# Performance work log

Hardware: AMD Instinct MI355X
Metric: run time of the kernel (lower is better)

## Reference

```python
import jax, jax.numpy as jnp
import numpy as np
import math

B, T, C, H = 2, 2048, 1024, 16
HD = C // H  # head_dim = 64


def _rope_cos_sin(t, hd, base=10000.0):
    inv_freq = 1.0 / (base ** (jnp.arange(0, hd, 2, dtype=jnp.float32) / hd))
    freqs = jnp.arange(t, dtype=jnp.float32)[:, None] * inv_freq[None, :]  # [T, hd//2]
    emb = jnp.concatenate([freqs, freqs], axis=-1)  # [T, hd]
    return jnp.cos(emb)[None, None], jnp.sin(emb)[None, None]  # [1,1,T,hd]


def setup_inputs() -> dict:
    key = jax.random.key(0)
    k1, k2, k3 = jax.random.split(key, 3)
    x = jax.random.normal(k1, (B, T, C), dtype=jnp.float32)
    W_attn = jax.random.normal(k2, (C, 3 * C), dtype=jnp.float32) * (1.0 / math.sqrt(C))
    W_proj = jax.random.normal(k3, (C, C), dtype=jnp.float32) * (1.0 / math.sqrt(C))
    mask = jnp.tril(jnp.ones((T, T), dtype=bool))[None, None]  # causal [1,1,T,T]
    return {"x": x, "W_attn": W_attn, "W_proj": W_proj, "mask": mask}


def reference(x, W_attn, W_proj, mask):
    b, t, c = x.shape
    qkv = x @ W_attn  # [B,T,3C]
    q, k, v = jnp.split(qkv, 3, axis=-1)
    q = q.reshape(b, t, H, HD).transpose(0, 2, 1, 3)  # [B,H,T,HD]
    k = k.reshape(b, t, H, HD).transpose(0, 2, 1, 3)
    v = v.reshape(b, t, H, HD).transpose(0, 2, 1, 3)
    cos, sin = _rope_cos_sin(t, HD)
    # roll-based RoPE: x*cos + roll(x, 1, axis=-1)*sin
    q = q * cos + jnp.roll(q, 1, axis=-1) * sin
    k = k * cos + jnp.roll(k, 1, axis=-1) * sin
    scale = 1.0 / math.sqrt(HD)
    att = jnp.einsum('bhqd,bhkd->bhqk', q, k) * scale  # [B,H,T,T]
    att = jnp.where(mask, att, -jnp.inf)
    att = jax.nn.softmax(att, axis=-1)
    y = jnp.einsum('bhqk,bhkd->bhqd', att, v)
    y = y.transpose(0, 2, 1, 3).reshape(b, t, c)
    return y @ W_proj
```

## Files before the change

### kernel.cpp

```cpp
#include <hip/hip_runtime.h>


typedef __attribute__((ext_vector_type(8))) short short8;
typedef __attribute__((ext_vector_type(4))) float floatx4;

__device__ __forceinline__ ushort f2bf(float f) {
    unsigned x = __float_as_uint(f);
    x += 0x7fffu + ((x >> 16) & 1u);
    return (ushort)(x >> 16);
}
__device__ __forceinline__ float bf2f(ushort u) {
    return __uint_as_float(((unsigned)u) << 16);
}
__device__ __forceinline__ float exp2fast(float x) {
    float r;
    asm("v_exp_f32 %0, %1" : "=v"(r) : "v"(x));
    return r;
}
__device__ __forceinline__ unsigned cvtpk_bf16(float lo, float hi) {
    unsigned r;
    asm("v_cvt_pk_bf16_f32 %0, %1, %2" : "=v"(r) : "v"(lo), "v"(hi));
    return r;
}

#define MFMA16(a, b, c) __builtin_amdgcn_mfma_f32_16x16x32_bf16((a), (b), (c), 0, 0, 0)

__device__ __forceinline__ void glds16(const ushort* g, ushort* l) {
    __builtin_amdgcn_global_load_lds(
        (const __attribute__((address_space(1))) unsigned int*)g,
        (__attribute__((address_space(3))) unsigned int*)l, 16, 0, 0);
}

__global__ __launch_bounds__(256) void tp_k(const float* __restrict__ src,
                                            ushort* __restrict__ dst,
                                            int R, int C) {
    __shared__ ushort t[32][34];
    const int c0 = blockIdx.x * 32, r0 = blockIdx.y * 32;
    const int tr = threadIdx.x >> 5, tc = threadIdx.x & 31;
#pragma unroll
    for (int j = 0; j < 4; j++)
        t[tr + j * 8][tc] = f2bf(src[(size_t)(r0 + tr + j * 8) * C + c0 + tc]);
    __syncthreads();
#pragma unroll
    for (int j = 0; j < 4; j++)
        dst[(size_t)(c0 + tr + j * 8) * R + r0 + tc] = t[tc][tr + j * 8];
}

__global__ __launch_bounds__(256) void cvt_k(const float* __restrict__ src,
                                             ushort* __restrict__ dst) {
    const size_t i = ((size_t)blockIdx.x * 256 + threadIdx.x) * 4;
    float4 t4 = *(const float4*)&src[i];
    *(ushort4*)&dst[i] = make_ushort4(f2bf(t4.x), f2bf(t4.y), f2bf(t4.z), f2bf(t4.w));
}

__global__ __launch_bounds__(256) void trig_k(float2* __restrict__ tab) {
    const int idx = blockIdx.x * 256 + threadIdx.x;
    const int t = idx >> 5, j = idx & 31;
    const double inv = pow(10000.0, -(double)j / 32.0);
    const double ang = (double)t * inv;
    tab[idx] = make_float2((float)cos(ang), (float)sin(ang));
}

__global__ __launch_bounds__(256, 3) void gemm1_qkv_k(const ushort* __restrict__ Ab,
                                                      const ushort* __restrict__ Bt,
                                                      ushort* __restrict__ qb,
                                                      ushort* __restrict__ kb,
                                                      ushort* __restrict__ vtb) {
    __shared__ __align__(16) ushort As[128 * 64];
    __shared__ __align__(16) ushort Bs[128 * 64];
    const size_t boff = (size_t)blockIdx.z * (2048u * 1024u);
    Ab += boff; qb += boff; kb += boff; vtb += boff;
    const int tid = threadIdx.x;
    const int m0 = blockIdx.y * 128, n0 = blockIdx.x * 128;
    const int w = tid >> 6, lane = tid & 63, quad = lane >> 4, l16 = lane & 15;
    const int wr = w >> 1, wc = w & 1;
    const int K = 1024;
    const int srow = lane >> 3, sslot = lane & 7;

    floatx4 acc[4][4];
#pragma unroll
    for (int mt = 0; mt < 4; mt++)
#pragma unroll
        for (int nt = 0; nt < 4; nt++) acc[mt][nt] = (floatx4){0.f, 0.f, 0.f, 0.f};

    for (int k0 = 0; k0 < K; k0 += 64) {
        __syncthreads();
#pragma unroll
        for (int jj = 0; jj < 4; jj++) {
            const int reg = jj * 4 + w;
            const int row = reg * 8 + srow;
            const int cs = sslot ^ (row & 7);
            glds16(&Ab[(size_t)(m0 + row) * K + k0 + cs * 8], &As[reg * 512]);
        }
#pragma unroll
        for (int jj = 0; jj < 4; jj++) {
            const int reg = jj * 4 + w;
            const int row = reg * 8 + srow;
            const int cs = sslot ^ (row & 7);
            glds16(&Bt[(size_t)(n0 + row) * K + k0 + cs * 8], &Bs[reg * 512]);
        }
        __syncthreads();

#pragma unroll
        for (int kk = 0; kk < 2; kk++) {
            short8 af[4], bfr[4];
#pragma unroll
            for (int mt = 0; mt < 4; mt++) {
                const int row = wr * 64 + mt * 16 + l16;
                const int slot = ((kk << 2) | quad) ^ (row & 7);
                af[mt] = *(short8*)&As[row * 64 + slot * 8];
            }
#pragma unroll
            for (int nt = 0; nt < 4; nt++) {
                const int row = wc * 64 + nt * 16 + l16;
                const int slot = ((kk << 2) | quad) ^ (row & 7);
                bfr[nt] = *(short8*)&Bs[row * 64 + slot * 8];
            }
#pragma unroll
            for (int mt = 0; mt < 4; mt++)
#pragma unroll
                for (int nt = 0; nt < 4; nt++) acc[mt][nt] = MFMA16(af[mt], bfr[nt], acc[mt][nt]);
        }
    }

#pragma unroll
    for (int nt = 0; nt < 4; nt++) {
        const int n = n0 + wc * 64 + nt * 16 + l16;
        const int seg = n >> 10;
        const int cn = n & 1023;
        const int h = cn >> 6, d = cn & 63;
#pragma unroll
        for (int mt = 0; mt < 4; mt++) {
#pragma unroll
            for (int r = 0; r < 4; r++) {
                const int t = m0 + wr * 64 + mt * 16 + quad * 4 + r;
                const ushort v = f2bf(acc[mt][nt][r]);
                if (seg == 0)      qb[((size_t)h * 2048 + t) * 64 + d] = v;
                else if (seg == 1) kb[((size_t)h * 2048 + t) * 64 + d] = v;
                else               vtb[((size_t)h * 64 + d) * 2048 + t] = v;
            }
        }
    }
}

__global__ __launch_bounds__(256) void rope_k(ushort* __restrict__ q,
                                              ushort* __restrict__ k,
                                              const float2* __restrict__ tab) {
    const int wid = blockIdx.x * 4 + (threadIdx.x >> 6);
    const int lane = threadIdx.x & 63;
    const int t = wid & 2047;
    const float2 cs = tab[t * 32 + (lane & 31)];
    const float c = cs.x;
    const float s = cs.y;
    const size_t base = (size_t)wid * 64;

    float qv = bf2f(q[base + lane]);
    float qp = __shfl(qv, (lane + 63) & 63, 64);
    q[base + lane] = f2bf(qv * c + qp * s);

    float kv = bf2f(k[base + lane]);
    float kp = __shfl(kv, (lane + 63) & 63, 64);
    k[base + lane] = f2bf(kv * c + kp * s);
}

__global__ __launch_bounds__(256, 2) void attn_k(const ushort* __restrict__ q,
                                                 const ushort* __restrict__ k,
                                                 const ushort* __restrict__ vt,
                                                 ushort* __restrict__ y) {
    __shared__ __align__(16) ushort Ks[128 * 64];
    __shared__ __align__(16) ushort Vs[64 * 128];
    __shared__ __align__(16) ushort Ps[4][16][136];

    const int bid = blockIdx.x;
    const int b = bid >> 9;
    const int r9 = bid & 511;
    const int qt = (r9 < 256) ? (31 - (r9 >> 4)) : ((r9 >> 4) - 16);
    const int h = r9 & 15;
    const size_t boff = (size_t)b * (2048u * 1024u);
    q += boff; k += boff; vt += boff; y += boff;
    const int tid = threadIdx.x, w = tid >> 6, lane = tid & 63;
    const int quad = lane >> 4, l16 = lane & 15;
    const int srow8 = lane >> 3, sslot8 = lane & 7;
    const int srow4 = lane >> 4, sslot16 = lane & 15;

    const int q0 = qt * 64;
    const int qrow = q0 + w * 16 + l16;
    const int wrow0 = q0 + w * 16;
    const int nkt = (qt >> 1) + 1;
    const float SC = 0.125f * 1.44269504f;

    short8 qa0, qa1;
    {
        const ushort* qp = q + ((size_t)h * 2048 + qrow) * 64 + quad * 8;
        qa0 = *(const short8*)(qp);
        qa1 = *(const short8*)(qp + 32);
    }

    floatx4 O[4];
#pragma unroll
    for (int dt = 0; dt < 4; dt++) O[dt] = (floatx4){0.f, 0.f, 0.f, 0.f};
    float M = -30000.f, L = 0.f;

    for (int kt2 = 0; kt2 < nkt; kt2++) {
        const int kbase = kt2 * 128;
        __syncthreads();
#pragma unroll
        for (int jj = 0; jj < 4; jj++) {
            const int reg = jj * 4 + w;
            const int row = reg * 8 + srow8;
            const int cs = sslot8 ^ (row & 7);
            glds16(&k[((size_t)h * 2048 + kbase + row) * 64 + cs * 8], &Ks[reg * 512]);
        }
#pragma unroll
        for (int jj = 0; jj < 4; jj++) {
            const int reg = jj * 4 + w;
            const int row = reg * 4 + srow4;
            const int cs = sslot16 ^ (row & 15);
            glds16(&vt[((size_t)h * 64 + row) * 2048 + kbase + cs * 8], &Vs[reg * 512]);
        }
        __syncthreads();

        floatx4 s[8];
        __builtin_amdgcn_s_setprio(1);
#pragma unroll
        for (int nt = 0; nt < 8; nt++) {
            const int row = nt * 16 + l16;
            short8 ka0 = *(short8*)&Ks[row * 64 + ((quad ^ (row & 7)) * 8)];
            short8 ka1 = *(short8*)&Ks[row * 64 + (((4 | quad) ^ (row & 7)) * 8)];
            floatx4 z = (floatx4){0.f, 0.f, 0.f, 0.f};
            z = MFMA16(ka0, qa0, z);
            z = MFMA16(ka1, qa1, z);
            s[nt] = z;
        }
        __builtin_amdgcn_s_setprio(0);

        if (kbase + 127 <= wrow0) {
#pragma unroll
            for (int nt = 0; nt < 8; nt++)
#pragma unroll
                for (int r = 0; r < 4; r++) s[nt][r] *= SC;
        } else {
#pragma unroll
            for (int nt = 0; nt < 8; nt++)
#pragma unroll
                for (int r = 0; r < 4; r++) {
                    const int kidx = kbase + nt * 16 + quad * 4 + r;
                    const float vv = s[nt][r] * SC;
                    s[nt][r] = (kidx > qrow) ? -30000.f : vv;
                }
        }

        float mr[8];
#pragma unroll
        for (int nt = 0; nt < 8; nt++)
            mr[nt] = fmaxf(fmaxf(s[nt][0], s[nt][1]), fmaxf(s[nt][2], s[nt][3]));
        float mx = fmaxf(fmaxf(fmaxf(mr[0], mr[1]), fmaxf(mr[2], mr[3])),
                         fmaxf(fmaxf(mr[4], mr[5]), fmaxf(mr[6], mr[7])));
        mx = fmaxf(mx, __shfl_xor(mx, 16, 64));
        mx = fmaxf(mx, __shfl_xor(mx, 32, 64));

        if (!__all(mx <= M)) {
            const float Mn = fmaxf(M, mx);
            const float alpha = exp2fast(M - Mn);
            L *= alpha;
#pragma unroll
            for (int dt = 0; dt < 4; dt++) O[dt] *= alpha;
            M = Mn;
        }

        float sum = 0.f;
#pragma unroll
        for (int nt = 0; nt < 8; nt++)
#pragma unroll
            for (int r = 0; r < 4; r++) {
                const float pv = exp2fast(s[nt][r] - M);
                s[nt][r] = pv;
                sum += pv;
            }
        sum += __shfl_xor(sum, 16, 64);
        sum += __shfl_xor(sum, 32, 64);
        L += sum;

#pragma unroll
        for (int nt = 0; nt < 8; nt++) {
            uint2 pk2;
            pk2.x = cvtpk_bf16(s[nt][0], s[nt][1]);
            pk2.y = cvtpk_bf16(s[nt][2], s[nt][3]);
            *(uint2*)&Ps[w][l16][nt * 16 + quad * 4] = pk2;
        }

        short8 pb[4];
#pragma unroll
        for (int ks = 0; ks < 4; ks++)
            pb[ks] = *(short8*)&Ps[w][l16][ks * 32 + quad * 8];
        __builtin_amdgcn_s_setprio(1);
#pragma unroll
        for (int dt = 0; dt < 4; dt++) {
            const int row = dt * 16 + l16;
#pragma unroll
            for (int ks = 0; ks < 4; ks++) {
                const int cc = (ks * 4 + quad) ^ (row & 15);
                short8 va = *(short8*)&Vs[row * 128 + cc * 8];
                O[dt] = MFMA16(va, pb[ks], O[dt]);
            }
        }
        __builtin_amdgcn_s_setprio(0);
    }

    const float rl = 1.0f / L;
#pragma unroll
    for (int dt = 0; dt < 4; dt++) {
        ushort4 o4 = make_ushort4(f2bf(O[dt][0] * rl), f2bf(O[dt][1] * rl),
                                  f2bf(O[dt][2] * rl), f2bf(O[dt][3] * rl));
        *(ushort4*)&y[(size_t)qrow * 1024 + h * 64 + dt * 16 + quad * 4] = o4;
    }
}

__global__ __launch_bounds__(256, 2) void gemm2_proj_k(const ushort* __restrict__ Y,
                                                       const ushort* __restrict__ Bt,
                                                       float* __restrict__ out) {
    __shared__ __align__(16) ushort As[64 * 64];
    __shared__ __align__(16) ushort Bs[64 * 64];
    const size_t boff = (size_t)blockIdx.z * (2048u * 1024u);
    Y += boff; out += boff;
    const int tid = threadIdx.x;
    const int m0 = blockIdx.y * 64, n0 = blockIdx.x * 64;
    const int w = tid >> 6, lane = tid & 63, quad = lane >> 4, l16 = lane & 15;
    const int wr = w >> 1, wc = w & 1;
    const int K = 1024;
    const int srow = lane >> 3, sslot = lane & 7;

    floatx4 acc[2][2];
#pragma unroll
    for (int mt = 0; mt < 2; mt++)
#pragma unroll
        for (int nt = 0; nt < 2; nt++) acc[mt][nt] = (floatx4){0.f, 0.f, 0.f, 0.f};

    for (int k0 = 0; k0 < K; k0 += 64) {
        __syncthreads();
#pragma unroll
        for (int jj = 0; jj < 2; jj++) {
            const int reg = jj * 4 + w;
            const int row = reg * 8 + srow;
            const int cs = sslot ^ (row & 7);
            glds16(&Y[(size_t)(m0 + row) * K + k0 + cs * 8], &As[reg * 512]);
            glds16(&Bt[(size_t)(n0 + row) * K + k0 + cs * 8], &Bs[reg * 512]);
        }
        __syncthreads();

#pragma unroll
        for (int kk = 0; kk < 2; kk++) {
            short8 af[2], bfr[2];
#pragma unroll
            for (int mt = 0; mt < 2; mt++) {
                const int row = wr * 32 + mt * 16 + l16;
                const int slot = ((kk << 2) | quad) ^ (row & 7);
                af[mt] = *(short8*)&As[row * 64 + slot * 8];
            }
#pragma unroll
            for (int nt = 0; nt < 2; nt++) {
                const int row = wc * 32 + nt * 16 + l16;
                const int slot = ((kk << 2) | quad) ^ (row & 7);
                bfr[nt] = *(short8*)&Bs[row * 64 + slot * 8];
            }
#pragma unroll
            for (int mt = 0; mt < 2; mt++)
#pragma unroll
                for (int nt = 0; nt < 2; nt++) acc[mt][nt] = MFMA16(af[mt], bfr[nt], acc[mt][nt]);
        }
    }

#pragma unroll
    for (int mt = 0; mt < 2; mt++)
#pragma unroll
        for (int nt = 0; nt < 2; nt++) {
            const int n = n0 + wc * 32 + nt * 16 + l16;
#pragma unroll
            for (int r = 0; r < 4; r++) {
                const int m = m0 + wr * 32 + mt * 16 + quad * 4 + r;
                out[(size_t)m * 1024 + n] = acc[mt][nt][r];
            }
        }
}

extern "C" void kernel_launch(void* const* d_in, const int* in_sizes, int n_in,
                              void* d_out, int out_size, void* d_ws, size_t ws_size,
                              hipStream_t stream) {
    const float* x  = (const float*)d_in[0];
    const float* Wa = (const float*)d_in[1];
    const float* Wp = (const float*)d_in[2];
    float* out = (float*)d_out;

    const size_t PB = (size_t)2048 * 1024;
    ushort* wtA = (ushort*)(out + PB);
    float2* tab = (float2*)(wtA + (size_t)3 * 1024 * 1024);

    if (ws_size >= (size_t)36 * 1024 * 1024) {
        ushort* qbA = (ushort*)d_ws;
        ushort* kbA = qbA + 2 * PB;
        ushort* vtA = qbA + 4 * PB;
        ushort* ybA = qbA + 6 * PB;
        ushort* wtP = qbA + 8 * PB;

        tp_k<<<dim3(96, 32), 256, 0, stream>>>(Wa, wtA, 1024, 3072);
        trig_k<<<dim3(256), 256, 0, stream>>>(tab);
        tp_k<<<dim3(32, 32), 256, 0, stream>>>(Wp, wtP, 1024, 1024);

        cvt_k<<<dim3(4096), 256, 0, stream>>>(x, ybA);
        gemm1_qkv_k<<<dim3(24, 16, 2), 256, 0, stream>>>(ybA, wtA, qbA, kbA, vtA);
        rope_k<<<dim3(16384), 256, 0, stream>>>(qbA, kbA, tab);
        attn_k<<<dim3(1024), 256, 0, stream>>>(qbA, kbA, vtA, ybA);
        gemm2_proj_k<<<dim3(16, 32, 2), 256, 0, stream>>>(ybA, wtP, out);
        return;
    }

    ushort* qb  = (ushort*)d_ws;
    ushort* kb  = qb + PB;
    ushort* vtb = kb + PB;
    ushort* yb  = vtb + PB;
    const bool hoistWp = ws_size >= (size_t)18 * 1024 * 1024;
    ushort* wtP_stable = yb + PB;

    tp_k<<<dim3(96, 32), 256, 0, stream>>>(Wa, wtA, 1024, 3072);
    trig_k<<<dim3(256), 256, 0, stream>>>(tab);
    if (hoistWp)
        tp_k<<<dim3(32, 32), 256, 0, stream>>>(Wp, wtP_stable, 1024, 1024);

    for (int b = 0; b < 2; b++) {
        cvt_k<<<dim3(2048), 256, 0, stream>>>(x + b * PB, yb);
        gemm1_qkv_k<<<dim3(24, 16, 1), 256, 0, stream>>>(yb, wtA, qb, kb, vtb);
        rope_k<<<dim3(8192), 256, 0, stream>>>(qb, kb, tab);
        attn_k<<<dim3(512), 256, 0, stream>>>(qb, kb, vtb, yb);
        if (hoistWp) {
            gemm2_proj_k<<<dim3(16, 32, 1), 256, 0, stream>>>(yb, wtP_stable, out + b * PB);
        } else {
            tp_k<<<dim3(32, 32), 256, 0, stream>>>(Wp, qb, 1024, 1024);
            gemm2_proj_k<<<dim3(16, 32, 1), 256, 0, stream>>>(yb, qb, out + b * PB);
        }
    }
}
```

Baseline: 204.1 us.

## Pair complementary causal query tiles per attention block to share K/V loads

Each attention workgroup now handles two query tiles, a late tile (31-g) and an early tile (g). Every K/V tile staged in shared memory is reused for both, and each block does a balanced amount of causal work. This halves the grid and cuts redundant K/V global loads for the early tile. In exchange it doubles the per-thread accumulator and Q registers, which may lower occupancy, and leaves fewer blocks (512) across the device's CUs.

```diff
diff --git a/kernel.cpp b/kernel.cpp
--- a/kernel.cpp
+++ b/kernel.cpp
@@ -172,10 +172,11 @@
     __shared__ __align__(16) ushort Ps[4][16][136];
 
     const int bid = blockIdx.x;
-    const int b = bid >> 9;
-    const int r9 = bid & 511;
-    const int qt = (r9 < 256) ? (31 - (r9 >> 4)) : ((r9 >> 4) - 16);
-    const int h = r9 & 15;
+    const int b = bid >> 8;
+    const int r8 = bid & 255;
+    const int g = r8 >> 4;
+    const int h = r8 & 15;
+    const int qtA = 31 - g, qtB = g;
     const size_t boff = (size_t)b * (2048u * 1024u);
     q += boff; k += boff; vt += boff; y += boff;
     const int tid = threadIdx.x, w = tid >> 6, lane = tid & 63;
@@ -183,25 +184,33 @@
     const int srow8 = lane >> 3, sslot8 = lane & 7;
     const int srow4 = lane >> 4, sslot16 = lane & 15;
 
-    const int q0 = qt * 64;
-    const int qrow = q0 + w * 16 + l16;
-    const int wrow0 = q0 + w * 16;
-    const int nkt = (qt >> 1) + 1;
+    const int qrowA = qtA * 64 + w * 16 + l16;
+    const int qrowB = qtB * 64 + w * 16 + l16;
+    const int wrow0A = qtA * 64 + w * 16;
+    const int wrow0B = qtB * 64 + w * 16;
+    const int nktA = (qtA >> 1) + 1;
+    const int nktB = (qtB >> 1) + 1;
     const float SC = 0.125f * 1.44269504f;
 
-    short8 qa0, qa1;
+    short8 qaA0, qaA1, qaB0, qaB1;
     {
-        const ushort* qp = q + ((size_t)h * 2048 + qrow) * 64 + quad * 8;
-        qa0 = *(const short8*)(qp);
-        qa1 = *(const short8*)(qp + 32);
-    }
-
-    floatx4 O[4];
-#pragma unroll
-    for (int dt = 0; dt < 4; dt++) O[dt] = (floatx4){0.f, 0.f, 0.f, 0.f};
-    float M = -30000.f, L = 0.f;
-
-    for (int kt2 = 0; kt2 < nkt; kt2++) {
+        const ushort* qp = q + ((size_t)h * 2048 + qrowA) * 64 + quad * 8;
+        qaA0 = *(const short8*)(qp);
+        qaA1 = *(const short8*)(qp + 32);
+        const ushort* qp2 = q + ((size_t)h * 2048 + qrowB) * 64 + quad * 8;
+        qaB0 = *(const short8*)(qp2);
+        qaB1 = *(const short8*)(qp2 + 32);
+    }
+
+    floatx4 OA[4], OB[4];
+#pragma unroll
+    for (int dt = 0; dt < 4; dt++) {
+        OA[dt] = (floatx4){0.f, 0.f, 0.f, 0.f};
+        OB[dt] = (floatx4){0.f, 0.f, 0.f, 0.f};
+    }
+    float MA = -30000.f, LA = 0.f, MB = -30000.f, LB = 0.f;
+
+    for (int kt2 = 0; kt2 < nktA; kt2++) {
         const int kbase = kt2 * 128;
         __syncthreads();
 #pragma unroll
@@ -220,99 +229,198 @@
         }
         __syncthreads();
 
-        floatx4 s[8];
-        __builtin_amdgcn_s_setprio(1);
-#pragma unroll
-        for (int nt = 0; nt < 8; nt++) {
-            const int row = nt * 16 + l16;
-            short8 ka0 = *(short8*)&Ks[row * 64 + ((quad ^ (row & 7)) * 8)];
-            short8 ka1 = *(short8*)&Ks[row * 64 + (((4 | quad) ^ (row & 7)) * 8)];
-            floatx4 z = (floatx4){0.f, 0.f, 0.f, 0.f};
-            z = MFMA16(ka0, qa0, z);
-            z = MFMA16(ka1, qa1, z);
-            s[nt] = z;
-        }
-        __builtin_amdgcn_s_setprio(0);
-
-        if (kbase + 127 <= wrow0) {
+        {
+            floatx4 s[8];
+            __builtin_amdgcn_s_setprio(1);
+#pragma unroll
+            for (int nt = 0; nt < 8; nt++) {
+                const int row = nt * 16 + l16;
+                short8 ka0 = *(short8*)&Ks[row * 64 + ((quad ^ (row & 7)) * 8)];
+                short8 ka1 = *(short8*)&Ks[row * 64 + (((4 | quad) ^ (row & 7)) * 8)];
+                floatx4 z = (floatx4){0.f, 0.f, 0.f, 0.f};
+                z = MFMA16(ka0, qaA0, z);
+                z = MFMA16(ka1, qaA1, z);
+                s[nt] = z;
+            }
+            __builtin_amdgcn_s_setprio(0);
+
+            if (kbase + 127 <= wrow0A) {
+#pragma unroll
+                for (int nt = 0; nt < 8; nt++)
+#pragma unroll
+                    for (int r = 0; r < 4; r++) s[nt][r] *= SC;
+            } else {
+#pragma unroll
+                for (int nt = 0; nt < 8; nt++)
+#pragma unroll
+                    for (int r = 0; r < 4; r++) {
+                        const int kidx = kbase + nt * 16 + quad * 4 + r;
+                        const float vv = s[nt][r] * SC;
+                        s[nt][r] = (kidx > qrowA) ? -30000.f : vv;
+                    }
+            }
+
+            float mr[8];
 #pragma unroll
             for (int nt = 0; nt < 8; nt++)
-#pragma unroll
-                for (int r = 0; r < 4; r++) s[nt][r] *= SC;
-        } else {
+                mr[nt] = fmaxf(fmaxf(s[nt][0], s[nt][1]), fmaxf(s[nt][2], s[nt][3]));
+            float mx = fmaxf(fmaxf(fmaxf(mr[0], mr[1]), fmaxf(mr[2], mr[3])),
+                             fmaxf(fmaxf(mr[4], mr[5]), fmaxf(mr[6], mr[7])));
+            mx = fmaxf(mx, __shfl_xor(mx, 16, 64));
+            mx = fmaxf(mx, __shfl_xor(mx, 32, 64));
+
+            if (!__all(mx <= MA)) {
+                const float Mn = fmaxf(MA, mx);
+                const float alpha = exp2fast(MA - Mn);
+                LA *= alpha;
+#pragma unroll
+                for (int dt = 0; dt < 4; dt++) OA[dt] *= alpha;
+                MA = Mn;
+            }
+
+            float sum = 0.f;
 #pragma unroll
             for (int nt = 0; nt < 8; nt++)
 #pragma unroll
                 for (int r = 0; r < 4; r++) {
-                    const int kidx = kbase + nt * 16 + quad * 4 + r;
-                    const float vv = s[nt][r] * SC;
-                    s[nt][r] = (kidx > qrow) ? -30000.f : vv;
+                    const float pv = exp2fast(s[nt][r] - MA);
+                    s[nt][r] = pv;
+                    sum += pv;
                 }
-        }
-
-        float mr[8];
-#pragma unroll
-        for (int nt = 0; nt < 8; nt++)
-            mr[nt] = fmaxf(fmaxf(s[nt][0], s[nt][1]), fmaxf(s[nt][2], s[nt][3]));
-        float mx = fmaxf(fmaxf(fmaxf(mr[0], mr[1]), fmaxf(mr[2], mr[3])),
-                         fmaxf(fmaxf(mr[4], mr[5]), fmaxf(mr[6], mr[7])));
-        mx = fmaxf(mx, __shfl_xor(mx, 16, 64));
-        mx = fmaxf(mx, __shfl_xor(mx, 32, 64));
-
-        if (!__all(mx <= M)) {
-            const float Mn = fmaxf(M, mx);
-            const float alpha = exp2fast(M - Mn);
-            L *= alpha;
-#pragma unroll
-            for (int dt = 0; dt < 4; dt++) O[dt] *= alpha;
-            M = Mn;
-        }
-
-        float sum = 0.f;
-#pragma unroll
-        for (int nt = 0; nt < 8; nt++)
-#pragma unroll
-            for (int r = 0; r < 4; r++) {
-                const float pv = exp2fast(s[nt][r] - M);
-                s[nt][r] = pv;
-                sum += pv;
-            }
-        sum += __shfl_xor(sum, 16, 64);
-        sum += __shfl_xor(sum, 32, 64);
-        L += sum;
-
-#pragma unroll
-        for (int nt = 0; nt < 8; nt++) {
-            uint2 pk2;
-            pk2.x = cvtpk_bf16(s[nt][0], s[nt][1]);
-            pk2.y = cvtpk_bf16(s[nt][2], s[nt][3]);
-            *(uint2*)&Ps[w][l16][nt * 16 + quad * 4] = pk2;
-        }
-
-        short8 pb[4];
-#pragma unroll
-        for (int ks = 0; ks < 4; ks++)
-            pb[ks] = *(short8*)&Ps[w][l16][ks * 32 + quad * 8];
-        __builtin_amdgcn_s_setprio(1);
+            sum += __shfl_xor(sum, 16, 64);
+            sum += __shfl_xor(sum, 32, 64);
+            LA += sum;
+
+#pragma unroll
+            for (int nt = 0; nt < 8; nt++) {
+                uint2 pk2;
+                pk2.x = cvtpk_bf16(s[nt][0], s[nt][1]);
+                pk2.y = cvtpk_bf16(s[nt][2], s[nt][3]);
+                *(uint2*)&Ps[w][l16][nt * 16 + quad * 4] = pk2;
+            }
+            short8 pb[4];
+#pragma unroll
+            for (int ks = 0; ks < 4; ks++)
+                pb[ks] = *(short8*)&Ps[w][l16][ks * 32 + quad * 8];
+            __builtin_amdgcn_s_setprio(1);
+#pragma unroll
+            for (int dt = 0; dt < 4; dt++) {
+                const int row = dt * 16 + l16;
+#pragma unroll
+                for (int ks = 0; ks < 4; ks++) {
+                    const int cc = (ks * 4 + quad) ^ (row & 15);
+                    short8 va = *(short8*)&Vs[row * 128 + cc * 8];
+                    OA[dt] = MFMA16(va, pb[ks], OA[dt]);
+                }
+            }
+            __builtin_amdgcn_s_setprio(0);
+        }
+
+        if (kt2 < nktB) {
+            floatx4 s[8];
+            __builtin_amdgcn_s_setprio(1);
+#pragma unroll
+            for (int nt = 0; nt < 8; nt++) {
+                const int row = nt * 16 + l16;
+                short8 ka0 = *(short8*)&Ks[row * 64 + ((quad ^ (row & 7)) * 8)];
+                short8 ka1 = *(short8*)&Ks[row * 64 + (((4 | quad) ^ (row & 7)) * 8)];
+                floatx4 z = (floatx4){0.f, 0.f, 0.f, 0.f};
+                z = MFMA16(ka0, qaB0, z);
+                z = MFMA16(ka1, qaB1, z);
+                s[nt] = z;
+            }
+            __builtin_amdgcn_s_setprio(0);
+
+            if (kbase + 127 <= wrow0B) {
+#pragma unroll
+                for (int nt = 0; nt < 8; nt++)
+#pragma unroll
+                    for (int r = 0; r < 4; r++) s[nt][r] *= SC;
+            } else {
+#pragma unroll
+                for (int nt = 0; nt < 8; nt++)
+#pragma unroll
+                    for (int r = 0; r < 4; r++) {
+                        const int kidx = kbase + nt * 16 + quad * 4 + r;
+                        const float vv = s[nt][r] * SC;
+                        s[nt][r] = (kidx > qrowB) ? -30000.f : vv;
+                    }
+            }
+
+            float mr[8];
+#pragma unroll
+            for (int nt = 0; nt < 8; nt++)
+                mr[nt] = fmaxf(fmaxf(s[nt][0], s[nt][1]), fmaxf(s[nt][2], s[nt][3]));
+            float mx = fmaxf(fmaxf(fmaxf(mr[0], mr[1]), fmaxf(mr[2], mr[3])),
+                             fmaxf(fmaxf(mr[4], mr[5]), fmaxf(mr[6], mr[7])));
+            mx = fmaxf(mx, __shfl_xor(mx, 16, 64));
+            mx = fmaxf(mx, __shfl_xor(mx, 32, 64));
+
+            if (!__all(mx <= MB)) {
+                const float Mn = fmaxf(MB, mx);
+                const float alpha = exp2fast(MB - Mn);
+                LB *= alpha;
+#pragma unroll
+                for (int dt = 0; dt < 4; dt++) OB[dt] *= alpha;
+                MB = Mn;
+            }
+
+            float sum = 0.f;
+#pragma unroll
+            for (int nt = 0; nt < 8; nt++)
+#pragma unroll
+                for (int r = 0; r < 4; r++) {
+                    const float pv = exp2fast(s[nt][r] - MB);
+                    s[nt][r] = pv;
+                    sum += pv;
+                }
+            sum += __shfl_xor(sum, 16, 64);
+            sum += __shfl_xor(sum, 32, 64);
+            LB += sum;
+
+#pragma unroll
+            for (int nt = 0; nt < 8; nt++) {
+                uint2 pk2;
+                pk2.x = cvtpk_bf16(s[nt][0], s[nt][1]);
+                pk2.y = cvtpk_bf16(s[nt][2], s[nt][3]);
+                *(uint2*)&Ps[w][l16][nt * 16 + quad * 4] = pk2;
+            }
+            short8 pb[4];
+#pragma unroll
+            for (int ks = 0; ks < 4; ks++)
+                pb[ks] = *(short8*)&Ps[w][l16][ks * 32 + quad * 8];
+            __builtin_amdgcn_s_setprio(1);
+#pragma unroll
+            for (int dt = 0; dt < 4; dt++) {
+                const int row = dt * 16 + l16;
+#pragma unroll
+                for (int ks = 0; ks < 4; ks++) {
+                    const int cc = (ks * 4 + quad) ^ (row & 15);
+                    short8 va = *(short8*)&Vs[row * 128 + cc * 8];
+                    OB[dt] = MFMA16(va, pb[ks], OB[dt]);
+                }
+            }
+            __builtin_amdgcn_s_setprio(0);
+        }
+    }
+
+    {
+        const float rl = 1.0f / LA;
 #pragma unroll
         for (int dt = 0; dt < 4; dt++) {
-            const int row = dt * 16 + l16;
-#pragma unroll
-            for (int ks = 0; ks < 4; ks++) {
-                const int cc = (ks * 4 + quad) ^ (row & 15);
-                short8 va = *(short8*)&Vs[row * 128 + cc * 8];
-                O[dt] = MFMA16(va, pb[ks], O[dt]);
-            }
-        }
-        __builtin_amdgcn_s_setprio(0);
-    }
-
-    const float rl = 1.0f / L;
-#pragma unroll
-    for (int dt = 0; dt < 4; dt++) {
-        ushort4 o4 = make_ushort4(f2bf(O[dt][0] * rl), f2bf(O[dt][1] * rl),
-                                  f2bf(O[dt][2] * rl), f2bf(O[dt][3] * rl));
-        *(ushort4*)&y[(size_t)qrow * 1024 + h * 64 + dt * 16 + quad * 4] = o4;
+            ushort4 o4 = make_ushort4(f2bf(OA[dt][0] * rl), f2bf(OA[dt][1] * rl),
+                                      f2bf(OA[dt][2] * rl), f2bf(OA[dt][3] * rl));
+            *(ushort4*)&y[(size_t)qrowA * 1024 + h * 64 + dt * 16 + quad * 4] = o4;
+        }
+    }
+    {
+        const float rl = 1.0f / LB;
+#pragma unroll
+        for (int dt = 0; dt < 4; dt++) {
+            ushort4 o4 = make_ushort4(f2bf(OB[dt][0] * rl), f2bf(OB[dt][1] * rl),
+                                      f2bf(OB[dt][2] * rl), f2bf(OB[dt][3] * rl));
+            *(ushort4*)&y[(size_t)qrowB * 1024 + h * 64 + dt * 16 + quad * 4] = o4;
+        }
     }
 }
 
@@ -409,7 +517,7 @@
         cvt_k<<<dim3(4096), 256, 0, stream>>>(x, ybA);
         gemm1_qkv_k<<<dim3(24, 16, 2), 256, 0, stream>>>(ybA, wtA, qbA, kbA, vtA);
         rope_k<<<dim3(16384), 256, 0, stream>>>(qbA, kbA, tab);
-        attn_k<<<dim3(1024), 256, 0, stream>>>(qbA, kbA, vtA, ybA);
+        attn_k<<<dim3(512), 256, 0, stream>>>(qbA, kbA, vtA, ybA);
         gemm2_proj_k<<<dim3(16, 32, 2), 256, 0, stream>>>(ybA, wtP, out);
         return;
     }
@@ -430,7 +538,7 @@
         cvt_k<<<dim3(2048), 256, 0, stream>>>(x + b * PB, yb);
         gemm1_qkv_k<<<dim3(24, 16, 1), 256, 0, stream>>>(yb, wtA, qb, kb, vtb);
         rope_k<<<dim3(8192), 256, 0, stream>>>(qb, kb, tab);
-        attn_k<<<dim3(512), 256, 0, stream>>>(qb, kb, vtb, yb);
+        attn_k<<<dim3(256), 256, 0, stream>>>(qb, kb, vtb, yb);
         if (hoistWp) {
             gemm2_proj_k<<<dim3(16, 32, 1), 256, 0, stream>>>(yb, wtP_stable, out + b * PB);
         } else {
```

Result: faster. 199.6 us (-2.2%).
